# Kernel optimization log

Hardware: AMD Instinct MI355X
Metric: run time of the kernel (lower is better)

The kernel has to match this reference:

```python
import jax, jax.numpy as jnp
import numpy as np

N, CH, K, B = 30000, 96, 81, 8
HIDDEN = max(CH // 4, 8)
EPS = 1e-5


def setup_inputs() -> dict:
    key = jax.random.key(0)
    ks = jax.random.split(key, 12)
    feats = jax.random.normal(ks[0], (N, CH), dtype=jnp.float32)
    nbr_idx = jax.random.randint(ks[1], (N, K), 0, N).astype(jnp.int32)
    batch_ids = jnp.sort(jax.random.randint(ks[2], (N,), 0, B)).astype(jnp.int32)
    s = 1.0 / np.sqrt(CH * 1.0)
    W1 = jax.random.normal(ks[3], (K, CH, CH), dtype=jnp.float32) * s
    W2 = jax.random.normal(ks[4], (K, CH, CH), dtype=jnp.float32) * s
    g1 = jnp.ones((CH,), jnp.float32); b1 = jnp.zeros((CH,), jnp.float32)
    g2 = jnp.ones((CH,), jnp.float32); b2 = jnp.zeros((CH,), jnp.float32)
    fc1_w = jax.random.normal(ks[5], (CH, HIDDEN), dtype=jnp.float32) * s
    fc1_b = jnp.zeros((HIDDEN,), jnp.float32)
    fc2_w = jax.random.normal(ks[6], (HIDDEN, CH), dtype=jnp.float32) * (1.0 / np.sqrt(HIDDEN * 1.0))
    fc2_b = jnp.zeros((CH,), jnp.float32)
    return {"feats": feats, "W1": W1, "g1": g1, "b1": b1, "W2": W2,
            "g2": g2, "b2": b2, "fc1_w": fc1_w, "fc1_b": fc1_b,
            "fc2_w": fc2_w, "fc2_b": fc2_b, "nbr_idx": nbr_idx,
            "batch_ids": batch_ids}


def _sparse_conv(x, W, nbr):
    # gather-matmul-scatter form of MinkowskiConvolution (kernel map shared):
    # g: [N, K, ch] gathered neighbor features; contract each offset's [ch,ch] weight.
    g = x[nbr]
    return jnp.einsum('nkc,kcd->nd', g, W)


def _bn(x, gamma, beta):
    mu = jnp.mean(x, axis=0)
    var = jnp.var(x, axis=0)
    return gamma * (x - mu) * jax.lax.rsqrt(var + EPS) + beta


def _se(x, batch_ids, fc1_w, fc1_b, fc2_w, fc2_b):
    # MinkowskiGlobalAvgPooling: per-sample mean over points
    sums = jax.ops.segment_sum(x, batch_ids, num_segments=B)
    cnts = jax.ops.segment_sum(jnp.ones((x.shape[0], 1), x.dtype), batch_ids, num_segments=B)
    pooled = sums / jnp.maximum(cnts, 1.0)  # [B, ch]
    w = jax.nn.relu(pooled @ fc1_w + fc1_b)
    w = jax.nn.sigmoid(w @ fc2_w + fc2_b)   # [B, ch]
    return x * w[batch_ids]                  # broadcast multiplication


def reference(feats, W1, g1, b1, W2, g2, b2, fc1_w, fc1_b, fc2_w, fc2_b,
              nbr_idx, batch_ids):
    out = jax.nn.relu(_bn(_sparse_conv(feats, W1, nbr_idx), g1, b1))
    out = _bn(_sparse_conv(out, W2, nbr_idx), g2, b2)
    out = _se(out, batch_ids, fc1_w, fc1_b, fc2_w, fc2_b)
    return jax.nn.relu(out + feats)
```

## Files before the change

kernel.cpp:

```cpp
#include <hip/hip_runtime.h>
#include <hip/hip_bf16.h>

#define NPTS 30000
#define CH 96
#define KOFF 81
#define NB 8
#define HID 24
#define EPSV 1e-5f
#define NTILE 469
#define RT 3
#define RSPLIT 157
#define KSPLIT 8

typedef __attribute__((ext_vector_type(8))) short bf16x8;
typedef __attribute__((ext_vector_type(4))) float f32x4;

__device__ __forceinline__ ushort f2bf(float f) {
    union { float f; unsigned int u; } x; x.f = f;
    unsigned int u = x.u;
    unsigned int r = (u + 0x7fffu + ((u >> 16) & 1u)) >> 16;
    return (ushort)r;
}

__device__ __forceinline__ void gll16(const void* g, void* l) {
    __builtin_amdgcn_global_load_lds(
        (const __attribute__((address_space(1))) unsigned int*)g,
        (__attribute__((address_space(3))) unsigned int*)l, 16, 0, 0);
}

__device__ __forceinline__ void bn_coeffs(const float* __restrict__ ssum,
                                          const float* __restrict__ ssq,
                                          const float* __restrict__ g,
                                          const float* __restrict__ b,
                                          float* s_scale, float* s_shift) {
    int t = threadIdx.x;
    if (t < 96) {
        float mean = ssum[t] * (1.0f / NPTS);
        float var = ssq[t] * (1.0f / NPTS) - mean * mean;
        float sc = g[t] * rsqrtf(var + EPSV);
        s_scale[t] = sc;
        s_shift[t] = b[t] - mean * sc;
    }
    __syncthreads();
}

__global__ __launch_bounds__(256) void k_prep(const float* __restrict__ feats,
                                              const float* __restrict__ W1,
                                              const float* __restrict__ W2,
                                              const int* __restrict__ nbr,
                                              ushort* __restrict__ featsbf,
                                              float* __restrict__ outbuf,
                                              int* __restrict__ nbrT,
                                              ushort* __restrict__ wt1,
                                              ushort* __restrict__ wt2) {
    __shared__ __align__(16) char smem[36864];
    int bid = blockIdx.x, tid = threadIdx.x;
    if (bid < 2813) {
        int t = bid * 256 + tid;
        if (t < 720000) {
            float4 v = reinterpret_cast<const float4*>(feats)[t];
            ushort4 o;
            o.x = f2bf(v.x); o.y = f2bf(v.y); o.z = f2bf(v.z); o.w = f2bf(v.w);
            reinterpret_cast<ushort4*>(featsbf)[t] = o;
            float4 z = {0.f, 0.f, 0.f, 0.f};
            reinterpret_cast<float4*>(outbuf)[t] = z;
        }
    } else if (bid < 3282) {
        int* lds = (int*)smem;
        int n0 = (bid - 2813) * 64;
        int rows = min(64, NPTS - n0);
        int cnt = rows * 81;
        for (int i = tid; i < cnt; i += 256) lds[i] = nbr[n0 * 81 + i];
        __syncthreads();
        for (int o = tid; o < cnt; o += 256) {
            int kk = o / rows, r = o - kk * rows;
            nbrT[kk * NPTS + n0 + r] = lds[r * 81 + kk];
        }
    } else {
        float* lds = (float*)smem;
        int b = bid - 3282;
        int k = (b < 81) ? b : b - 81;
        const float* src = ((b < 81) ? W1 : W2) + k * 9216;
        ushort* dst = ((b < 81) ? wt1 : wt2) + k * 9216;
        for (int j = tid; j < 9216; j += 256) lds[j] = src[j];
        __syncthreads();
        for (int o = tid; o < 9216; o += 256) {
            int q = o / 768, rem = o - q * 768, d = rem >> 3, j = rem & 7;
            dst[o] = f2bf(lds[(q * 8 + j) * 96 + d]);
        }
    }
}

__global__ __launch_bounds__(256, 3) void k_conv(const ushort* __restrict__ xbf,
                                                 const ushort* __restrict__ wt,
                                                 const int* __restrict__ nbrT,
                                                 float* __restrict__ out) {
    __shared__ __align__(16) ushort Wsm[2][9216];

    const int tid = threadIdx.x;
    const int slice = blockIdx.x / RSPLIT;
    const int rb = blockIdx.x % RSPLIT;
    const int k0 = slice * 10;
    const int k1 = k0 + ((slice == 7) ? 11 : 10);
    const int wave = tid >> 6, lane = tid & 63;
    const int r16 = lane & 15, kg = lane >> 4;
    const int tile0 = rb * RT;

    int nrow[RT];
#pragma unroll
    for (int rt = 0; rt < RT; ++rt) {
        int n = (tile0 + rt) * 64 + wave * 16 + r16;
        nrow[rt] = (n < NPTS) ? n : (NPTS - 1);
    }

    f32x4 zero4 = {0.f, 0.f, 0.f, 0.f};
    f32x4 acc[RT][6];
#pragma unroll
    for (int rt = 0; rt < RT; ++rt)
#pragma unroll
        for (int db = 0; db < 6; ++db) acc[rt][db] = zero4;

    {
        const ushort* wsrc = wt + k0 * 9216 + lane * 8;
#pragma unroll
        for (int t = 0; t < 5; ++t) {
            int i = wave + t * 4;
            if (i < 18) gll16(wsrc + i * 512, Wsm[0] + i * 512);
        }
    }
    int idx[RT];
#pragma unroll
    for (int rt = 0; rt < RT; ++rt) idx[rt] = nbrT[k0 * NPTS + nrow[rt]];
    __syncthreads();

    int cur = 0;
    for (int k = k0; k < k1; ++k) {
        bf16x8 afrag[RT][3];
#pragma unroll
        for (int rt = 0; rt < RT; ++rt) {
            const ushort* as = xbf + idx[rt] * 96 + kg * 8;
#pragma unroll
            for (int c = 0; c < 3; ++c)
                afrag[rt][c] = *reinterpret_cast<const bf16x8*>(as + c * 32);
        }
        if (k + 1 < k1) {
            const ushort* wsrc = wt + (k + 1) * 9216 + lane * 8;
#pragma unroll
            for (int t = 0; t < 5; ++t) {
                int i = wave + t * 4;
                if (i < 18) gll16(wsrc + i * 512, Wsm[cur ^ 1] + i * 512);
            }
#pragma unroll
            for (int rt = 0; rt < RT; ++rt) idx[rt] = nbrT[(k + 1) * NPTS + nrow[rt]];
        }
#pragma unroll
        for (int c = 0; c < 3; ++c) {
            const int q = c * 4 + kg;
            bf16x8 bfrag[6];
#pragma unroll
            for (int db = 0; db < 6; ++db)
                bfrag[db] = *reinterpret_cast<const bf16x8*>(
                    &Wsm[cur][q * 768 + (db * 16 + r16) * 8]);
#pragma unroll
            for (int rt = 0; rt < RT; ++rt)
#pragma unroll
                for (int db = 0; db < 6; ++db)
                    acc[rt][db] = __builtin_amdgcn_mfma_f32_16x16x32_bf16(
                        afrag[rt][c], bfrag[db], acc[rt][db], 0, 0, 0);
        }
        __syncthreads();
        cur ^= 1;
    }

#pragma unroll
    for (int rt = 0; rt < RT; ++rt) {
        int rbase = (tile0 + rt) * 64 + wave * 16 + kg * 4;
#pragma unroll
        for (int db = 0; db < 6; ++db) {
            int col = db * 16 + r16;
#pragma unroll
            for (int i = 0; i < 4; ++i) {
                int r = rbase + i;
                if (r < NPTS) atomicAdd(&out[r * 96 + col], acc[rt][db][i]);
            }
        }
    }
}

__device__ __forceinline__ int lowb(const int* __restrict__ bids, int v) {
    int lo = 0, hi = NPTS;
    while (lo < hi) { int m = (lo + hi) >> 1; if (bids[m] < v) lo = m + 1; else hi = m; }
    return lo;
}

template <bool SEG>
__global__ __launch_bounds__(256) void k_stats(const float* __restrict__ y,
                                               const int* __restrict__ bids,
                                               float* __restrict__ ssum,
                                               float* __restrict__ ssq,
                                               float* __restrict__ segsum,
                                               float* __restrict__ cntf) {
    __shared__ float ls[96], lq[96], lg[96];
    int tid = threadIdx.x;
    if (tid < 96) { ls[tid] = 0.f; lq[tid] = 0.f; lg[tid] = 0.f; }
    __syncthreads();

    int b = 0, j, s, e;
    if (SEG) {
        b = blockIdx.x >> 5; j = blockIdx.x & 31;
        s = lowb(bids, b); e = lowb(bids, b + 1);
    } else {
        j = blockIdx.x; s = 0; e = NPTS;
    }
    const int stride = SEG ? (32 * 256) : (256 * 256);
    const int total = (e - s) * 24;
    const int base4 = s * 24;
    const int c40 = j * 256 + tid;

    f32x4 z = {0.f, 0.f, 0.f, 0.f};
    f32x4 sm[3] = {z, z, z}, sq[3] = {z, z, z};
    for (int c4 = c40; c4 < total; c4 += 3 * stride) {
#pragma unroll
        for (int m = 0; m < 3; ++m) {
            int c = c4 + m * stride;
            if (c < total) {
                f32x4 v = reinterpret_cast<const f32x4*>(y)[base4 + c];
                sm[m] += v; sq[m] += v * v;
            }
        }
    }
#pragma unroll
    for (int m = 0; m < 3; ++m) {
        int d0 = ((c40 + m * stride) * 4) % 96;
#pragma unroll
        for (int w = 0; w < 4; ++w) {
            atomicAdd(&ls[d0 + w], sm[m][w]);
            atomicAdd(&lq[d0 + w], sq[m][w]);
            if (SEG) atomicAdd(&lg[d0 + w], sm[m][w]);
        }
    }
    __syncthreads();
    if (tid < 96) {
        atomicAdd(&ssum[tid], ls[tid]);
        atomicAdd(&ssq[tid], lq[tid]);
        if (SEG) atomicAdd(&segsum[b * 96 + tid], lg[tid]);
    }
    if (SEG && tid == 0 && (blockIdx.x & 31) == 0) cntf[b] = (float)(e - s);
}

__global__ void k_apply1(float* __restrict__ x,
                         const float* __restrict__ ssum, const float* __restrict__ ssq,
                         const float* __restrict__ g, const float* __restrict__ b,
                         ushort* __restrict__ h) {
    __shared__ float scale[96], shift[96];
    bn_coeffs(ssum, ssq, g, b, scale, shift);
    int t = blockIdx.x * 256 + threadIdx.x;
    if (t >= 720000) return;
    float4 v = reinterpret_cast<const float4*>(x)[t];
    int d0 = (t * 4) % 96;
    ushort4 o;
    o.x = f2bf(fmaxf(v.x * scale[d0] + shift[d0], 0.f));
    o.y = f2bf(fmaxf(v.y * scale[d0 + 1] + shift[d0 + 1], 0.f));
    o.z = f2bf(fmaxf(v.z * scale[d0 + 2] + shift[d0 + 2], 0.f));
    o.w = f2bf(fmaxf(v.w * scale[d0 + 3] + shift[d0 + 3], 0.f));
    reinterpret_cast<ushort4*>(h)[t] = o;
    float4 z = {0.f, 0.f, 0.f, 0.f};
    reinterpret_cast<float4*>(x)[t] = z;
}

__global__ void k_se(const float* __restrict__ segsum, const float* __restrict__ cnt,
                     const float* __restrict__ ssum, const float* __restrict__ ssq,
                     const float* __restrict__ g, const float* __restrict__ b,
                     const float* __restrict__ fc1w, const float* __restrict__ fc1b,
                     const float* __restrict__ fc2w, const float* __restrict__ fc2b,
                     float* __restrict__ sew) {
    __shared__ float scale[96], shift[96];
    __shared__ float pooled[NB][96];
    __shared__ float hid[NB][HID];
    bn_coeffs(ssum, ssq, g, b, scale, shift);
    int t = threadIdx.x;
    for (int i = t; i < NB * 96; i += 256) {
        int bb = i / 96, d = i - bb * 96;
        pooled[bb][d] = segsum[i] / fmaxf(cnt[bb], 1.f) * scale[d] + shift[d];
    }
    __syncthreads();
    if (t < NB * HID) {
        int bb = t / HID, h = t - bb * HID;
        float s = fc1b[h];
        for (int d = 0; d < 96; ++d) s += pooled[bb][d] * fc1w[d * HID + h];
        hid[bb][h] = fmaxf(s, 0.f);
    }
    __syncthreads();
    for (int i = t; i < NB * 96; i += 256) {
        int bb = i / 96, d = i - bb * 96;
        float s = fc2b[d];
        for (int h = 0; h < HID; ++h) s += hid[bb][h] * fc2w[h * 96 + d];
        sew[i] = 1.f / (1.f + expf(-s));
    }
}

__global__ void k_final(const float* __restrict__ out2, const float* __restrict__ feats,
                        const float* __restrict__ ssum, const float* __restrict__ ssq,
                        const float* __restrict__ g, const float* __restrict__ b,
                        const float* __restrict__ sew, const int* __restrict__ bids,
                        float* __restrict__ out) {
    __shared__ float scale[96], shift[96];
    bn_coeffs(ssum, ssq, g, b, scale, shift);
    int t = blockIdx.x * 256 + threadIdx.x;
    if (t >= 720000) return;
    int e0 = t * 4;
    int n = e0 / 96;
    int d0 = e0 - n * 96;
    int bb = bids[n];
    const float* w = sew + bb * 96;
    float4 v = reinterpret_cast<const float4*>(out2)[t];
    float4 f = reinterpret_cast<const float4*>(feats)[t];
    float4 o;
    o.x = fmaxf((v.x * scale[d0] + shift[d0]) * w[d0] + f.x, 0.f);
    o.y = fmaxf((v.y * scale[d0 + 1] + shift[d0 + 1]) * w[d0 + 1] + f.y, 0.f);
    o.z = fmaxf((v.z * scale[d0 + 2] + shift[d0 + 2]) * w[d0 + 2] + f.z, 0.f);
    o.w = fmaxf((v.w * scale[d0 + 3] + shift[d0 + 3]) * w[d0 + 3] + f.w, 0.f);
    reinterpret_cast<float4*>(out)[t] = o;
}


extern "C" void kernel_launch(void* const* d_in, const int* in_sizes, int n_in,
                              void* d_out, int out_size, void* d_ws, size_t ws_size,
                              hipStream_t stream) {
    const float* feats = (const float*)d_in[0];
    const float* W1 = (const float*)d_in[1];
    const float* g1 = (const float*)d_in[2];
    const float* b1 = (const float*)d_in[3];
    const float* W2 = (const float*)d_in[4];
    const float* g2 = (const float*)d_in[5];
    const float* b2 = (const float*)d_in[6];
    const float* fc1w = (const float*)d_in[7];
    const float* fc1b = (const float*)d_in[8];
    const float* fc2w = (const float*)d_in[9];
    const float* fc2b = (const float*)d_in[10];
    const int* nbr = (const int*)d_in[11];
    const int* bids = (const int*)d_in[12];
    float* out = (float*)d_out;

    char* ws = (char*)d_ws;
    ushort* featsbf = (ushort*)(ws + 0);
    ushort* wt1 = (ushort*)(ws + 5760000);
    ushort* wt2 = (ushort*)(ws + 7252992);
    int* nbrT = (int*)(ws + 8745984);
    float* outbuf = (float*)(ws + 18465984);
    ushort* h1bf = (ushort*)(ws + 29985984);
    float* small = (float*)(ws + 35745984);
    float* sum1 = small + 0;
    float* sq1 = small + 96;
    float* sum2 = small + 192;
    float* sq2 = small + 288;
    float* segsum = small + 768;
    float* cntf = small + 1536;
    float* sew = small + 1544;

    const int gE = 2813;
    const int gC = KSPLIT * RSPLIT;

    hipMemsetAsync(small, 0, 16384, stream);
    k_prep<<<3444, 256, 0, stream>>>(feats, W1, W2, nbr, featsbf, outbuf, nbrT, wt1, wt2);

    k_conv<<<gC, 256, 0, stream>>>(featsbf, wt1, nbrT, outbuf);
    k_stats<false><<<256, 256, 0, stream>>>(outbuf, bids, sum1, sq1, segsum, cntf);
    k_apply1<<<gE, 256, 0, stream>>>(outbuf, sum1, sq1, g1, b1, h1bf);

    k_conv<<<gC, 256, 0, stream>>>(h1bf, wt2, nbrT, outbuf);
    k_stats<true><<<256, 256, 0, stream>>>(outbuf, bids, sum2, sq2, segsum, cntf);

    k_se<<<1, 256, 0, stream>>>(segsum, cntf, sum2, sq2, g2, b2, fc1w, fc1b, fc2w, fc2b, sew);
    k_final<<<gE, 256, 0, stream>>>(outbuf, feats, sum2, sq2, g2, b2, sew, bids, out);
}
```

Before: 382.6 us.

## Use single-wave conv blocks reading weights directly from global memory

The sparse conv kernel changes from 256-thread blocks that double-buffer each offset's weight slab in LDS into 64-thread single-wave blocks. Each block handles 48 rows and reads weight fragments straight from global/L2. The K dimension is split into 4 slices of about 20 offsets instead of 8 of about 10, which halves the atomicAdd traffic into the output. This removes LDS staging and per-offset barriers. In exchange, weight reuse across waves is lost, so each wave re-fetches the full weight slab from cache.

```diff
diff --git a/kernel.cpp b/kernel.cpp
--- a/kernel.cpp
+++ b/kernel.cpp
@@ -7,10 +7,9 @@
 #define NB 8
 #define HID 24
 #define EPSV 1e-5f
-#define NTILE 469
 #define RT 3
-#define RSPLIT 157
-#define KSPLIT 8
+#define GSPLIT 625
+#define KSPLIT 4
 
 typedef __attribute__((ext_vector_type(8))) short bf16x8;
 typedef __attribute__((ext_vector_type(4))) float f32x4;
@@ -20,12 +19,6 @@
     unsigned int u = x.u;
     unsigned int r = (u + 0x7fffu + ((u >> 16) & 1u)) >> 16;
     return (ushort)r;
-}
-
-__device__ __forceinline__ void gll16(const void* g, void* l) {
-    __builtin_amdgcn_global_load_lds(
-        (const __attribute__((address_space(1))) unsigned int*)g,
-        (__attribute__((address_space(3))) unsigned int*)l, 16, 0, 0);
 }
 
 __device__ __forceinline__ void bn_coeffs(const float* __restrict__ ssum,
@@ -91,27 +84,17 @@
     }
 }
 
-__global__ __launch_bounds__(256, 3) void k_conv(const ushort* __restrict__ xbf,
-                                                 const ushort* __restrict__ wt,
-                                                 const int* __restrict__ nbrT,
-                                                 float* __restrict__ out) {
-    __shared__ __align__(16) ushort Wsm[2][9216];
-
-    const int tid = threadIdx.x;
-    const int slice = blockIdx.x / RSPLIT;
-    const int rb = blockIdx.x % RSPLIT;
-    const int k0 = slice * 10;
-    const int k1 = k0 + ((slice == 7) ? 11 : 10);
-    const int wave = tid >> 6, lane = tid & 63;
+__global__ __launch_bounds__(64) void k_conv(const ushort* __restrict__ xbf,
+                                             const ushort* __restrict__ wt,
+                                             const int* __restrict__ nbrT,
+                                             float* __restrict__ out) {
+    const int lane = threadIdx.x;
+    const int slice = blockIdx.x / GSPLIT;
+    const int g = blockIdx.x % GSPLIT;
+    const int k0 = slice * 20;
+    const int k1 = k0 + ((slice == 3) ? 21 : 20);
     const int r16 = lane & 15, kg = lane >> 4;
-    const int tile0 = rb * RT;
-
-    int nrow[RT];
-#pragma unroll
-    for (int rt = 0; rt < RT; ++rt) {
-        int n = (tile0 + rt) * 64 + wave * 16 + r16;
-        nrow[rt] = (n < NPTS) ? n : (NPTS - 1);
-    }
+    const int row0 = g * 48;
 
     f32x4 zero4 = {0.f, 0.f, 0.f, 0.f};
     f32x4 acc[RT][6];
@@ -120,20 +103,10 @@
 #pragma unroll
         for (int db = 0; db < 6; ++db) acc[rt][db] = zero4;
 
-    {
-        const ushort* wsrc = wt + k0 * 9216 + lane * 8;
-#pragma unroll
-        for (int t = 0; t < 5; ++t) {
-            int i = wave + t * 4;
-            if (i < 18) gll16(wsrc + i * 512, Wsm[0] + i * 512);
-        }
-    }
     int idx[RT];
 #pragma unroll
-    for (int rt = 0; rt < RT; ++rt) idx[rt] = nbrT[k0 * NPTS + nrow[rt]];
-    __syncthreads();
-
-    int cur = 0;
+    for (int rt = 0; rt < RT; ++rt) idx[rt] = nbrT[k0 * NPTS + row0 + rt * 16 + r16];
+
     for (int k = k0; k < k1; ++k) {
         bf16x8 afrag[RT][3];
 #pragma unroll
@@ -144,15 +117,11 @@
                 afrag[rt][c] = *reinterpret_cast<const bf16x8*>(as + c * 32);
         }
         if (k + 1 < k1) {
-            const ushort* wsrc = wt + (k + 1) * 9216 + lane * 8;
-#pragma unroll
-            for (int t = 0; t < 5; ++t) {
-                int i = wave + t * 4;
-                if (i < 18) gll16(wsrc + i * 512, Wsm[cur ^ 1] + i * 512);
-            }
-#pragma unroll
-            for (int rt = 0; rt < RT; ++rt) idx[rt] = nbrT[(k + 1) * NPTS + nrow[rt]];
-        }
+#pragma unroll
+            for (int rt = 0; rt < RT; ++rt)
+                idx[rt] = nbrT[(k + 1) * NPTS + row0 + rt * 16 + r16];
+        }
+        const ushort* wk = wt + k * 9216;
 #pragma unroll
         for (int c = 0; c < 3; ++c) {
             const int q = c * 4 + kg;
@@ -160,7 +129,7 @@
 #pragma unroll
             for (int db = 0; db < 6; ++db)
                 bfrag[db] = *reinterpret_cast<const bf16x8*>(
-                    &Wsm[cur][q * 768 + (db * 16 + r16) * 8]);
+                    wk + q * 768 + (db * 16 + r16) * 8);
 #pragma unroll
             for (int rt = 0; rt < RT; ++rt)
 #pragma unroll
@@ -168,21 +137,17 @@
                     acc[rt][db] = __builtin_amdgcn_mfma_f32_16x16x32_bf16(
                         afrag[rt][c], bfrag[db], acc[rt][db], 0, 0, 0);
         }
-        __syncthreads();
-        cur ^= 1;
     }
 
 #pragma unroll
     for (int rt = 0; rt < RT; ++rt) {
-        int rbase = (tile0 + rt) * 64 + wave * 16 + kg * 4;
+        int rbase = row0 + rt * 16 + kg * 4;
 #pragma unroll
         for (int db = 0; db < 6; ++db) {
             int col = db * 16 + r16;
 #pragma unroll
-            for (int i = 0; i < 4; ++i) {
-                int r = rbase + i;
-                if (r < NPTS) atomicAdd(&out[r * 96 + col], acc[rt][db][i]);
-            }
+            for (int i = 0; i < 4; ++i)
+                atomicAdd(&out[(rbase + i) * 96 + col], acc[rt][db][i]);
         }
     }
 }
@@ -359,16 +324,16 @@
     float* sew = small + 1544;
 
     const int gE = 2813;
-    const int gC = KSPLIT * RSPLIT;
+    const int gC = KSPLIT * GSPLIT;
 
     hipMemsetAsync(small, 0, 16384, stream);
     k_prep<<<3444, 256, 0, stream>>>(feats, W1, W2, nbr, featsbf, outbuf, nbrT, wt1, wt2);
 
-    k_conv<<<gC, 256, 0, stream>>>(featsbf, wt1, nbrT, outbuf);
+    k_conv<<<gC, 64, 0, stream>>>(featsbf, wt1, nbrT, outbuf);
     k_stats<false><<<256, 256, 0, stream>>>(outbuf, bids, sum1, sq1, segsum, cntf);
     k_apply1<<<gE, 256, 0, stream>>>(outbuf, sum1, sq1, g1, b1, h1bf);
 
-    k_conv<<<gC, 256, 0, stream>>>(h1bf, wt2, nbrT, outbuf);
+    k_conv<<<gC, 64, 0, stream>>>(h1bf, wt2, nbrT, outbuf);
     k_stats<true><<<256, 256, 0, stream>>>(outbuf, bids, sum2, sq2, segsum, cntf);
 
     k_se<<<1, 256, 0, stream>>>(segsum, cntf, sum2, sq2, g2, b2, fc1w, fc1b, fc2w, fc2b, sew);
```

New measurement: 364.6 us. 4.7% less time.
